# Kernel tuning notes

Measured on AMD Instinct MI355X. Metric: run time of the kernel, lower is better.

## Reference

```python
import jax, jax.numpy as jnp
import numpy as np

B, T, C = 2, 2048, 2048
H, HD = 16, 128          # n_head, head_dim
DC, DC1 = 672, 672        # kv / q compression dims
DR = 64                   # decoupled rope dim
DN = HD - DR              # nope dim = 64
GATE_CH = 32


def _rope(x, cos, sin):
    # x: (B,T,h,D); cos/sin: (B,T,D//2) -> broadcast over heads
    cos = cos[:, :, None, :]
    sin = sin[:, :, None, :]
    d = x.shape[-1] // 2
    x1, x2 = x[..., :d], x[..., d:]
    return jnp.concatenate([x1 * cos + x2 * sin, -x1 * sin + x2 * cos], axis=-1)


def _rmsnorm(x):
    eps = jnp.finfo(x.dtype).eps
    return x * jax.lax.rsqrt(jnp.mean(jnp.square(x), axis=-1, keepdims=True) + eps)


def setup_inputs() -> dict:
    key = jax.random.key(0)
    ks = jax.random.split(key, 10)
    x = jax.random.normal(ks[0], (B, T, C), jnp.float32)
    ve = jax.random.normal(ks[1], (B, T, H * HD), jnp.float32)
    # rotary tables for d_rope//2 = 32 frequencies
    inv_freq = 1.0 / (10000.0 ** (jnp.arange(DR // 2, dtype=jnp.float32) / (DR // 2)))
    ang = jnp.arange(T, dtype=jnp.float32)[:, None] * inv_freq[None, :]  # (T, DR//2)
    cos = jnp.broadcast_to(jnp.cos(ang)[None], (B, T, DR // 2)).astype(jnp.float32)
    sin = jnp.broadcast_to(jnp.sin(ang)[None], (B, T, DR // 2)).astype(jnp.float32)
    s = 0.02
    w_dkv = s * jax.random.normal(ks[2], (C, DC), jnp.float32)
    w_ukv = s * jax.random.normal(ks[3], (DC, H * (DN + HD)), jnp.float32)
    w_kr = s * jax.random.normal(ks[4], (C, DR), jnp.float32)
    w_dq = s * jax.random.normal(ks[5], (C, DC1), jnp.float32)
    w_q = s * jax.random.normal(ks[6], (DC1, H * HD), jnp.float32)
    w_cproj = s * jax.random.normal(ks[7], (H * HD, C), jnp.float32)
    w_ve_gate = s * jax.random.normal(ks[8], (GATE_CH, H), jnp.float32)
    return {"x": x, "ve": ve, "cos": cos, "sin": sin,
            "w_dkv": w_dkv, "w_ukv": w_ukv, "w_kr": w_kr, "w_dq": w_dq,
            "w_q": w_q, "w_cproj": w_cproj, "w_ve_gate": w_ve_gate,
            "window_size": 0}


def reference(x, ve, cos, sin, w_dkv, w_ukv, w_kr, w_dq, w_q, w_cproj, w_ve_gate, window_size):
    b, t, _ = x.shape
    # low-rank KV path
    c_kv = x @ w_dkv                                   # (B,T,DC)
    kv = (c_kv @ w_ukv).reshape(b, t, H, DN + HD)
    k_nope, v = kv[..., :DN], kv[..., DN:]
    # decoupled rope key (single shared head)
    k_rope = (x @ w_kr).reshape(b, t, 1, DR)
    k_rope = _rope(k_rope, cos, sin)
    # value-embedding gate
    gate = 2.0 * jax.nn.sigmoid(x[..., :GATE_CH] @ w_ve_gate)   # (B,T,H)
    v = v + gate[..., None] * ve.reshape(b, t, H, HD)
    # low-rank Q path
    q = ((x @ w_dq) @ w_q).reshape(b, t, H, HD)
    q_nope, q_rope = q[..., :DN], q[..., DN:]
    q_rope = _rope(q_rope, cos, sin)
    k = jnp.concatenate([k_nope, jnp.broadcast_to(k_rope, (b, t, H, DR))], axis=-1)
    q = jnp.concatenate([q_nope, q_rope], axis=-1)
    q, k = _rmsnorm(q), _rmsnorm(k)
    # causal attention (window_size==0 -> full causal, matching window_size=(-1,-1))
    scale = 1.0 / jnp.sqrt(jnp.float32(HD))
    scores = jnp.einsum('bqhd,bkhd->bhqk', q, k) * scale
    causal = jnp.tril(jnp.ones((t, t), dtype=bool))
    scores = jnp.where(causal[None, None], scores, jnp.finfo(scores.dtype).min)
    att = jax.nn.softmax(scores, axis=-1)
    y = jnp.einsum('bhqk,bkhd->bqhd', att, v).reshape(b, t, H * HD)
    return y @ w_cproj
```

## Files before the change

### kernel.cpp

```cpp
#include <hip/hip_runtime.h>
#include <hip/hip_bf16.h>

typedef unsigned short u16;
typedef unsigned int u32;
typedef __bf16 bf16x8 __attribute__((ext_vector_type(8)));
typedef float f32x4 __attribute__((ext_vector_type(4)));
typedef u16 ushort8 __attribute__((ext_vector_type(8)));

#define TSEQ 2048
#define NHEAD 16

#define GLD16(gp, lp) __builtin_amdgcn_global_load_lds( \
    (__attribute__((address_space(1))) void*)(gp), \
    (__attribute__((address_space(3))) void*)(lp), 16, 0, 0)

static __device__ __forceinline__ float bf2f(u16 u) {
  unsigned int x = ((unsigned int)u) << 16;
  union { unsigned int i; float f; } c; c.i = x; return c.f;
}
static __device__ __forceinline__ u16 f2bf(float f) {
  union { float f; unsigned int i; } c; c.f = f;
  unsigned int x = c.i;
  unsigned int r = (x + 0x7FFFu + ((x >> 16) & 1u)) >> 16;
  return (u16)r;
}
static __device__ __forceinline__ void st_out(u16* p, float v) { *p = f2bf(v); }
static __device__ __forceinline__ void st_out(float* p, float v) { *p = v; }
static __device__ __forceinline__ u32 cvtpk(float lo, float hi) {
  u32 w;
  asm("v_cvt_pk_bf16_f32 %0, %1, %2" : "=v"(w) : "v"(lo), "v"(hi));
  return w;
}

__global__ __launch_bounds__(256) void k_conv_x(const float* __restrict__ x, u16* __restrict__ xb) {
  size_t i = ((size_t)blockIdx.x * 256 + threadIdx.x) * 8;
  float4 a = *(const float4*)(x + i);
  float4 b = *(const float4*)(x + i + 4);
  ushort8 o;
  o[0] = f2bf(a.x); o[1] = f2bf(a.y); o[2] = f2bf(a.z); o[3] = f2bf(a.w);
  o[4] = f2bf(b.x); o[5] = f2bf(b.y); o[6] = f2bf(b.z); o[7] = f2bf(b.w);
  *(ushort8*)(xb + i) = o;
}

__global__ __launch_bounds__(256) void k_tconv_all(const float* __restrict__ w_dkv, const float* __restrict__ w_dq,
                                                   const float* __restrict__ w_kr, const float* __restrict__ w_ukv,
                                                   const float* __restrict__ w_q, const float* __restrict__ w_cp,
                                                   u16* __restrict__ wcatT, u16* __restrict__ wukvT,
                                                   u16* __restrict__ wqT, u16* __restrict__ wcpT) {
  __shared__ float sm[32][33];
  int z = blockIdx.x;
  const float* src; u16* dst; int R, Cc, Rpad, bx, by;
  if (z < 1536)       { src = w_dkv; dst = wcatT;              R = 2048; Cc = 672;  Rpad = 2048; int l = z;        bx = l % 64; by = l / 64; }
  else if (z < 3072)  { src = w_dq;  dst = wcatT + 768 * 2048; R = 2048; Cc = 672;  Rpad = 2048; int l = z - 1536; bx = l % 64; by = l / 64; }
  else if (z < 3200)  { src = w_kr;  dst = wcatT + 1536 * 2048;R = 2048; Cc = 64;   Rpad = 2048; int l = z - 3072; bx = l % 64; by = l / 64; }
  else if (z < 5504)  { src = w_ukv; dst = wukvT;              R = 672;  Cc = 3072; Rpad = 768;  int l = z - 3200; bx = l % 24; by = l / 24; }
  else if (z < 7040)  { src = w_q;   dst = wqT;                R = 672;  Cc = 2048; Rpad = 768;  int l = z - 5504; bx = l % 24; by = l / 24; }
  else                { src = w_cp;  dst = wcpT;               R = 2048; Cc = 2048; Rpad = 2048; int l = z - 7040; bx = l % 64; by = l / 64; }
  int tx = threadIdx.x & 31, ty = threadIdx.x >> 5;
  int r0 = bx * 32, c0 = by * 32;
#pragma unroll
  for (int i = 0; i < 4; i++) {
    int r = r0 + ty + 8 * i;
    int c = c0 + tx;
    sm[ty + 8 * i][tx] = (r < R && c < Cc) ? src[(size_t)r * Cc + c] : 0.f;
  }
  __syncthreads();
#pragma unroll
  for (int i = 0; i < 4; i++) {
    int c = c0 + ty + 8 * i;
    dst[(size_t)c * Rpad + r0 + tx] = f2bf(sm[tx][ty + 8 * i]);
  }
}

__global__ __launch_bounds__(256) void k_gate(const float* __restrict__ x, const float* __restrict__ wg,
                                              float* __restrict__ gate) {
  int idx = blockIdx.x * 256 + threadIdx.x;
  int m = idx >> 4, h = idx & 15;
  const float* xr = x + (size_t)m * 2048;
  float s = 0.f;
#pragma unroll
  for (int j = 0; j < 32; j++) s += xr[j] * wg[j * 16 + h];
  gate[idx] = 2.f / (1.f + __expf(-s));
}

template <typename OT>
__global__ __launch_bounds__(256) void k_gemm128(const u16* __restrict__ A, int lda,
                                                 const u16* __restrict__ BT, int ldb,
                                                 OT* __restrict__ C, int ldc,
                                                 int K) {
  __shared__ __align__(16) u16 As[128 * 32];
  __shared__ __align__(16) u16 Bs[128 * 32];
  int t = threadIdx.x;
  int wid = t >> 6, lane = t & 63;
  int m0 = blockIdx.y * 128, n0 = blockIdx.x * 128;
  int c0 = wid * 2;
  int srow0 = c0 * 16 + (lane >> 2);
  int scol = (lane & 3) * 8;
  const u16* Ag0 = A + (size_t)(m0 + srow0) * lda + scol;
  const u16* Ag1 = A + (size_t)(m0 + srow0 + 16) * lda + scol;
  const u16* Bg0 = BT + (size_t)(n0 + srow0) * ldb + scol;
  const u16* Bg1 = BT + (size_t)(n0 + srow0 + 16) * ldb + scol;
  u16* Al0 = &As[c0 * 512];
  u16* Al1 = &As[c0 * 512 + 512];
  u16* Bl0 = &Bs[c0 * 512];
  u16* Bl1 = &Bs[c0 * 512 + 512];
  int wr = (wid >> 1) * 64, wc = (wid & 1) * 64;
  int fr = lane & 15, fo = (lane >> 4) * 8;
  f32x4 acc[4][4];
#pragma unroll
  for (int m = 0; m < 4; m++)
#pragma unroll
    for (int n = 0; n < 4; n++) acc[m][n] = (f32x4){0, 0, 0, 0};
  for (int k0 = 0; k0 < K; k0 += 32) {
    GLD16(Ag0 + k0, Al0);
    GLD16(Ag1 + k0, Al1);
    GLD16(Bg0 + k0, Bl0);
    GLD16(Bg1 + k0, Bl1);
    __syncthreads();
    bf16x8 af[4], bf[4];
#pragma unroll
    for (int m = 0; m < 4; m++) af[m] = *(const bf16x8*)&As[(wr + m * 16 + fr) * 32 + fo];
#pragma unroll
    for (int n = 0; n < 4; n++) bf[n] = *(const bf16x8*)&Bs[(wc + n * 16 + fr) * 32 + fo];
#pragma unroll
    for (int m = 0; m < 4; m++)
#pragma unroll
      for (int n = 0; n < 4; n++)
        acc[m][n] = __builtin_amdgcn_mfma_f32_16x16x32_bf16(af[m], bf[n], acc[m][n], 0, 0, 0);
    __syncthreads();
  }
  int cr = (lane >> 4) * 4, cc = lane & 15;
#pragma unroll
  for (int m = 0; m < 4; m++)
#pragma unroll
    for (int n = 0; n < 4; n++)
#pragma unroll
      for (int r = 0; r < 4; r++)
        st_out(&C[(size_t)(m0 + wr + m * 16 + cr + r) * ldc + n0 + wc + n * 16 + cc], acc[m][n][r]);
}

__global__ __launch_bounds__(256) void k_gemm_dual(const u16* __restrict__ catout,
                                                   const u16* __restrict__ wukvT,
                                                   u16* __restrict__ kvb,
                                                   const u16* __restrict__ wqT,
                                                   const float* __restrict__ cosp,
                                                   const float* __restrict__ sinp,
                                                   u16* __restrict__ qf) {
  __shared__ __align__(16) u16 As[128 * 32];
  __shared__ __align__(16) u16 Bs[128 * 32];
  int t = threadIdx.x;
  int wid = t >> 6, lane = t & 63;
  int bx = blockIdx.x;
  bool isq = (bx >= 24);
  int nx = isq ? bx - 24 : bx;
  int m0 = blockIdx.y * 128, n0 = nx * 128;
  const u16* A = isq ? catout + 768 : catout;
  const u16* BT = isq ? wqT : wukvT;
  int c0 = wid * 2;
  int srow0 = c0 * 16 + (lane >> 2);
  int scol = (lane & 3) * 8;
  const u16* Ag0 = A + (size_t)(m0 + srow0) * 1664 + scol;
  const u16* Ag1 = A + (size_t)(m0 + srow0 + 16) * 1664 + scol;
  const u16* Bg0 = BT + (size_t)(n0 + srow0) * 768 + scol;
  const u16* Bg1 = BT + (size_t)(n0 + srow0 + 16) * 768 + scol;
  u16* Al0 = &As[c0 * 512];
  u16* Al1 = &As[c0 * 512 + 512];
  u16* Bl0 = &Bs[c0 * 512];
  u16* Bl1 = &Bs[c0 * 512 + 512];
  int wr = (wid >> 1) * 64, wc = (wid & 1) * 64;
  int fr = lane & 15, fo = (lane >> 4) * 8;
  f32x4 acc[4][4];
#pragma unroll
  for (int m = 0; m < 4; m++)
#pragma unroll
    for (int n = 0; n < 4; n++) acc[m][n] = (f32x4){0, 0, 0, 0};
  for (int k0 = 0; k0 < 768; k0 += 32) {
    GLD16(Ag0 + k0, Al0);
    GLD16(Ag1 + k0, Al1);
    GLD16(Bg0 + k0, Bl0);
    GLD16(Bg1 + k0, Bl1);
    __syncthreads();
    bf16x8 af[4], bf[4];
#pragma unroll
    for (int m = 0; m < 4; m++) af[m] = *(const bf16x8*)&As[(wr + m * 16 + fr) * 32 + fo];
#pragma unroll
    for (int n = 0; n < 4; n++) bf[n] = *(const bf16x8*)&Bs[(wc + n * 16 + fr) * 32 + fo];
#pragma unroll
    for (int m = 0; m < 4; m++)
#pragma unroll
      for (int n = 0; n < 4; n++)
        acc[m][n] = __builtin_amdgcn_mfma_f32_16x16x32_bf16(af[m], bf[n], acc[m][n], 0, 0, 0);
    __syncthreads();
  }
  int cr = (lane >> 4) * 4, cc = lane & 15;
  if (!isq) {
#pragma unroll
    for (int m = 0; m < 4; m++)
#pragma unroll
      for (int n = 0; n < 4; n++)
#pragma unroll
        for (int r = 0; r < 4; r++)
          kvb[(size_t)(m0 + wr + m * 16 + cr + r) * 3072 + n0 + wc + n * 16 + cc] = f2bf(acc[m][n][r]);
    return;
  }
  int h = nx;
  int wch = wid & 1;
  int wrg = wid >> 1;
  if (wch == 1) {
#pragma unroll
    for (int m = 0; m < 4; m++)
#pragma unroll
      for (int r = 0; r < 4; r++) {
        int grow = m0 + wr + m * 16 + cr + r;
#pragma unroll
        for (int n = 0; n < 2; n++) {
          int i = n * 16 + cc;
          float cth = cosp[(size_t)grow * 32 + i];
          float sth = sinp[(size_t)grow * 32 + i];
          float x1 = acc[m][n][r], x2 = acc[m][n + 2][r];
          acc[m][n][r]     = x1 * cth + x2 * sth;
          acc[m][n + 2][r] = x2 * cth - x1 * sth;
        }
      }
  }
  float part[4][4];
#pragma unroll
  for (int m = 0; m < 4; m++)
#pragma unroll
    for (int r = 0; r < 4; r++) {
      float s2 = 0.f;
#pragma unroll
      for (int n = 0; n < 4; n++) s2 += acc[m][n][r] * acc[m][n][r];
#pragma unroll
      for (int o = 1; o < 16; o <<= 1) s2 += __shfl_xor(s2, o, 64);
      part[m][r] = s2;
    }
  float* xs = (float*)As;
  if (cc == 0) {
#pragma unroll
    for (int m = 0; m < 4; m++)
#pragma unroll
      for (int r = 0; r < 4; r++)
        xs[(wrg * 2 + wch) * 64 + m * 16 + cr + r] = part[m][r];
  }
  __syncthreads();
#pragma unroll
  for (int m = 0; m < 4; m++)
#pragma unroll
    for (int r = 0; r < 4; r++) {
      int lrow = m * 16 + cr + r;
      float tot = part[m][r] + xs[(wrg * 2 + (wch ^ 1)) * 64 + lrow];
      float rms = rsqrtf(tot * (1.f / 128.f) + 1.1920929e-7f) * 0.1275174245f;
      int grow = m0 + wr + lrow;
      int b2 = grow >> 11, tt = grow & 2047;
      size_t base = (((size_t)(b2 * NHEAD + h)) * TSEQ + tt) * 128 + wch * 64;
#pragma unroll
      for (int n = 0; n < 4; n++)
        qf[base + n * 16 + cc] = f2bf(acc[m][n][r] * rms);
    }
}

__global__ __launch_bounds__(256) void k_build_k(const u16* __restrict__ kv, const u16* __restrict__ kr,
                                                 const float* __restrict__ cosp, const float* __restrict__ sinp,
                                                 u16* __restrict__ ksw) {
  __shared__ __align__(16) u16 sm[8192];
  int tid = threadIdx.x, wid = tid >> 6, lane = tid & 63;
  int bh = blockIdx.x >> 5, tile = blockIdx.x & 31;
  int b = bh >> 4, h = bh & 15;
  int d0 = lane * 2;
  for (int rr = 0; rr < 16; rr++) {
    int row = wid * 16 + rr;
    int t = tile * 64 + row;
    int m = b * TSEQ + t;
    float v[2];
#pragma unroll
    for (int e = 0; e < 2; e++) {
      int d = d0 + e;
      float val;
      if (d < 64) {
        val = bf2f(kv[(size_t)m * 3072 + h * 192 + d]);
      } else {
        int dd = d - 64, i = dd & 31;
        float c = cosp[m * 32 + i], s = sinp[m * 32 + i];
        float x1 = bf2f(kr[(size_t)m * 1664 + i]), x2 = bf2f(kr[(size_t)m * 1664 + 32 + i]);
        val = (dd < 32) ? (x1 * c + x2 * s) : (x2 * c - x1 * s);
      }
      v[e] = val;
    }
    float ss = v[0] * v[0] + v[1] * v[1];
#pragma unroll
    for (int o = 1; o < 64; o <<= 1) ss += __shfl_xor(ss, o, 64);
    float rms = rsqrtf(ss * (1.f / 128.f) + 1.1920929e-7f);
    int a = (row * 256 + d0 * 2) ^ ((row & 7) << 4);
    sm[a >> 1] = f2bf(v[0] * rms);
    sm[(a >> 1) + 1] = f2bf(v[1] * rms);
  }
  __syncthreads();
  u16* dst = ksw + ((size_t)(bh * 32 + tile)) * 8192 + tid * 32;
  const u16* src = sm + tid * 32;
#pragma unroll
  for (int j = 0; j < 4; j++)
    *(ushort8*)(dst + j * 8) = *(const ushort8*)(src + j * 8);
}

__global__ __launch_bounds__(256) void k_build_v(const u16* __restrict__ kv, const float* __restrict__ ve,
                                                 const float* __restrict__ gate, u16* __restrict__ vsw) {
  __shared__ __align__(16) char sm[128 * 128];
  int bh = blockIdx.x >> 5, tile = blockIdx.x & 31;
  int t0 = tile * 64;
  int b = bh >> 4, h = bh & 15;
  int tt = threadIdx.x >> 2, dp = (threadIdx.x & 3) * 32;
  int m = b * TSEQ + t0 + tt;
  float g = gate[m * 16 + h];
  const u16* kvp = kv + (size_t)m * 3072 + h * 192 + 64 + dp;
  const float* vep = ve + (size_t)m * 2048 + h * 128 + dp;
  ushort8 kvv[4];
  float4 vev[8];
#pragma unroll
  for (int u = 0; u < 4; u++) kvv[u] = *(const ushort8*)(kvp + u * 8);
#pragma unroll
  for (int u = 0; u < 8; u++) vev[u] = *(const float4*)(vep + u * 4);
#pragma unroll
  for (int j = 0; j < 32; j++) {
    float vvf = ((const float*)&vev[j >> 2])[j & 3];
    float v = bf2f(kvv[j >> 3][j & 7]) + g * vvf;
    int row = dp + j;
    int a = row * 128 + tt * 2;
    *(u16*)(sm + (a ^ ((row & 7) << 4))) = f2bf(v);
  }
  __syncthreads();
  u16* dst = vsw + ((size_t)(bh * 32 + tile)) * 8192 + threadIdx.x * 32;
  const u16* src = (const u16*)sm + threadIdx.x * 32;
#pragma unroll
  for (int j = 0; j < 4; j++)
    *(ushort8*)(dst + j * 8) = *(const ushort8*)(src + j * 8);
}

__global__ __launch_bounds__(256, 2) void k_attn(const u16* __restrict__ qf, const u16* __restrict__ ksw,
                                                 const u16* __restrict__ vsw, u16* __restrict__ y,
                                                 float* __restrict__ opart, float* __restrict__ mpart,
                                                 float* __restrict__ lpart) {
  __shared__ __align__(16) u16 kvbuf[2][2][8192];
  __shared__ __align__(16) char plds_all[4][4096];
  int tid = threadIdx.x, wid = tid >> 6, lane = tid & 63;
  int gq = lane >> 4, c = lane & 15;
  int xcd = blockIdx.x & 7, r0r = blockIdx.x >> 3;
  int bh, qb, it0, it1, pidx = -1;
  if (r0r < 64) {
    bh = xcd * 4 + (r0r & 3);
    int sub = r0r >> 2;
    qb = 15 - (sub >> 1);
    int half = sub & 1;
    it0 = half ? (qb + 1) : 0;
    it1 = half ? (2 * qb + 2) : (qb + 1);
    pidx = bh * 16 + (qb - 8) * 2 + half;
  } else {
    int rr = r0r - 64;
    bh = xcd * 4 + (rr & 3);
    qb = 7 - (rr >> 2);
    it0 = 0;
    it1 = 2 * qb + 2;
  }
  int q0w = qb * 128 + wid * 32;
  const u16* qp = qf + (size_t)bh * TSEQ * 128;
  const u16* kswb = ksw + (size_t)bh * 32 * 8192;
  const u16* vswb = vsw + (size_t)bh * 32 * 8192;
  char* plds = plds_all[wid];
  int swz = (c & 7) << 4;
  bf16x8 qfr[2][4];
#pragma unroll
  for (int rg = 0; rg < 2; rg++)
#pragma unroll
    for (int kc = 0; kc < 4; kc++)
      qfr[rg][kc] = *(const bf16x8*)(qp + (size_t)(q0w + rg * 16 + c) * 128 + kc * 32 + gq * 8);
  f32x4 oacc[2][8];
#pragma unroll
  for (int rg = 0; rg < 2; rg++)
#pragma unroll
    for (int nd = 0; nd < 8; nd++) oacc[rg][nd] = (f32x4){0, 0, 0, 0};
  float mreg[2] = {-1e30f, -1e30f}, lreg[2] = {0.f, 0.f};
  int chunk = wid * 4;
#pragma unroll
  for (int j = 0; j < 4; j++) {
    GLD16(kswb + (size_t)it0 * 8192 + (chunk + j) * 512 + lane * 8, &kvbuf[0][0][(chunk + j) * 512]);
    GLD16(vswb + (size_t)it0 * 8192 + (chunk + j) * 512 + lane * 8, &kvbuf[0][1][(chunk + j) * 512]);
  }
  __syncthreads();
  for (int it = it0; it < it1; it++) {
    int cur = (it - it0) & 1;
    if (it + 1 < it1) {
      const u16* kt = kswb + (size_t)(it + 1) * 8192;
      const u16* vt = vswb + (size_t)(it + 1) * 8192;
#pragma unroll
      for (int j = 0; j < 4; j++) {
        GLD16(kt + (chunk + j) * 512 + lane * 8, &kvbuf[cur ^ 1][0][(chunk + j) * 512]);
        GLD16(vt + (chunk + j) * 512 + lane * 8, &kvbuf[cur ^ 1][1][(chunk + j) * 512]);
      }
    }
    int kt0 = it * 64;
    if (kt0 <= q0w + 31) {
      const char* Kt = (const char*)kvbuf[cur][0];
      const char* Vt = (const char*)kvbuf[cur][1];
      bool maskit = (kt0 + 63 > q0w);
      f32x4 sacc[2][4];
#pragma unroll
      for (int rg = 0; rg < 2; rg++)
#pragma unroll
        for (int s = 0; s < 4; s++) sacc[rg][s] = (f32x4){0, 0, 0, 0};
#pragma unroll
      for (int s = 0; s < 4; s++) {
        int row = s * 16 + c;
#pragma unroll
        for (int kc = 0; kc < 4; kc++) {
          int a = (row * 256 + (kc * 32 + gq * 8) * 2) ^ ((row & 7) << 4);
          bf16x8 kfr = *(const bf16x8*)(Kt + a);
          sacc[0][s] = __builtin_amdgcn_mfma_f32_16x16x32_bf16(kfr, qfr[0][kc], sacc[0][s], 0, 0, 0);
          sacc[1][s] = __builtin_amdgcn_mfma_f32_16x16x32_bf16(kfr, qfr[1][kc], sacc[1][s], 0, 0, 0);
        }
      }
      if (maskit) {
#pragma unroll
        for (int rg = 0; rg < 2; rg++) {
          int qrow = q0w + rg * 16 + c;
#pragma unroll
          for (int s = 0; s < 4; s++)
#pragma unroll
            for (int r = 0; r < 4; r++) {
              int key = kt0 + s * 16 + gq * 4 + r;
              sacc[rg][s][r] = (key <= qrow) ? sacc[rg][s][r] : -3e38f;
            }
        }
      }
      float mx[2];
#pragma unroll
      for (int rg = 0; rg < 2; rg++) {
        float m2 = sacc[rg][0][0];
#pragma unroll
        for (int s = 0; s < 4; s++)
#pragma unroll
          for (int r = 0; r < 4; r++) m2 = fmaxf(m2, sacc[rg][s][r]);
        m2 = fmaxf(m2, __shfl_xor(m2, 16, 64));
        m2 = fmaxf(m2, __shfl_xor(m2, 32, 64));
        mx[rg] = m2;
      }
      bool ok = (mx[0] - mreg[0] <= 11.f) && (mx[1] - mreg[1] <= 11.f);
      if (!__all(ok)) {
#pragma unroll
        for (int rg = 0; rg < 2; rg++) {
          float mn = fmaxf(mreg[rg], mx[rg]);
          float fac = exp2f(mreg[rg] - mn);
          lreg[rg] *= fac;
          float fq[4];
#pragma unroll
          for (int r = 0; r < 4; r++) fq[r] = __shfl(fac, gq * 4 + r, 64);
#pragma unroll
          for (int nd = 0; nd < 8; nd++)
#pragma unroll
            for (int r = 0; r < 4; r++) oacc[rg][nd][r] *= fq[r];
          mreg[rg] = mn;
        }
      }
#pragma unroll
      for (int rg = 0; rg < 2; rg++) {
        float p[4][4];
        float rs = 0.f;
#pragma unroll
        for (int s = 0; s < 4; s++)
#pragma unroll
          for (int r = 0; r < 4; r++) {
            p[s][r] = exp2f(sacc[rg][s][r] - mreg[rg]);
            rs += p[s][r];
          }
        rs += __shfl_xor(rs, 16, 64);
        rs += __shfl_xor(rs, 32, 64);
        lreg[rg] += rs;
#pragma unroll
        for (int s = 0; s < 4; s++) {
          u32 w0 = cvtpk(p[s][0], p[s][1]);
          u32 w1 = cvtpk(p[s][2], p[s][3]);
          int a = (rg * 2048 + c * 128 + s * 32 + gq * 8) ^ swz;
          *(uint2*)(plds + a) = make_uint2(w0, w1);
        }
      }
#pragma unroll
      for (int kc2 = 0; kc2 < 2; kc2++) {
        int a0 = (c * 128 + kc2 * 64 + gq * 16) ^ swz;
        bf16x8 pa0 = *(const bf16x8*)(plds + a0);
        bf16x8 pa1 = *(const bf16x8*)(plds + 2048 + a0);
#pragma unroll
        for (int nd = 0; nd < 8; nd++) {
          int vrow = nd * 16 + c;
          int av = (vrow * 128 + (kc2 * 32 + gq * 8) * 2) ^ ((vrow & 7) << 4);
          bf16x8 vfr = *(const bf16x8*)(Vt + av);
          oacc[0][nd] = __builtin_amdgcn_mfma_f32_16x16x32_bf16(pa0, vfr, oacc[0][nd], 0, 0, 0);
          oacc[1][nd] = __builtin_amdgcn_mfma_f32_16x16x32_bf16(pa1, vfr, oacc[1][nd], 0, 0, 0);
        }
      }
    }
    __syncthreads();
  }
  if (pidx >= 0) {
    float* op = opart + (size_t)pidx * 16384;
#pragma unroll
    for (int rg = 0; rg < 2; rg++) {
#pragma unroll
      for (int nd = 0; nd < 8; nd++)
#pragma unroll
        for (int r = 0; r < 4; r++)
          op[(wid * 32 + rg * 16 + gq * 4 + r) * 128 + nd * 16 + c] = oacc[rg][nd][r];
      if (gq == 0) {
        mpart[pidx * 128 + wid * 32 + rg * 16 + c] = mreg[rg];
        lpart[pidx * 128 + wid * 32 + rg * 16 + c] = lreg[rg];
      }
    }
    return;
  }
  int b2 = bh >> 4, h2 = bh & 15;
#pragma unroll
  for (int rg = 0; rg < 2; rg++) {
    float linv = 1.f / lreg[rg];
    float inv[4];
#pragma unroll
    for (int r = 0; r < 4; r++) inv[r] = __shfl(linv, gq * 4 + r, 64);
#pragma unroll
    for (int nd = 0; nd < 8; nd++) {
#pragma unroll
      for (int r = 0; r < 4; r++) {
        size_t offo = ((size_t)(b2 * TSEQ + q0w + rg * 16 + gq * 4 + r)) * 2048 + h2 * 128 + nd * 16 + c;
        y[offo] = f2bf(oacc[rg][nd][r] * inv[r]);
      }
    }
  }
}

__global__ __launch_bounds__(256) void k_merge(const float* __restrict__ opart, const float* __restrict__ mpart,
                                               const float* __restrict__ lpart, u16* __restrict__ y) {
  int blk = blockIdx.x;
  int bh = blk >> 3, qb = 8 + (blk & 7);
  int p0 = bh * 16 + (qb - 8) * 2, p1 = p0 + 1;
  int b2 = bh >> 4, h2 = bh & 15;
  for (int e = threadIdx.x; e < 16384; e += 256) {
    int row = e >> 7, col = e & 127;
    float m0 = mpart[p0 * 128 + row], m1 = mpart[p1 * 128 + row];
    float mm = fmaxf(m0, m1);
    float e0 = exp2f(m0 - mm), e1 = exp2f(m1 - mm);
    float l = lpart[p0 * 128 + row] * e0 + lpart[p1 * 128 + row] * e1;
    float o = opart[(size_t)p0 * 16384 + row * 128 + col] * e0 +
              opart[(size_t)p1 * 16384 + row * 128 + col] * e1;
    y[((size_t)(b2 * TSEQ + qb * 128 + row)) * 2048 + h2 * 128 + col] = f2bf(o / l);
  }
}

extern "C" void kernel_launch(void* const* d_in, const int* in_sizes, int n_in,
                              void* d_out, int out_size, void* d_ws, size_t ws_size,
                              hipStream_t stream) {
  (void)in_sizes; (void)n_in; (void)out_size; (void)ws_size;
  const float* x      = (const float*)d_in[0];
  const float* ve     = (const float*)d_in[1];
  const float* cosp   = (const float*)d_in[2];
  const float* sinp   = (const float*)d_in[3];
  const float* w_dkv  = (const float*)d_in[4];
  const float* w_ukv  = (const float*)d_in[5];
  const float* w_kr   = (const float*)d_in[6];
  const float* w_dq   = (const float*)d_in[7];
  const float* w_q    = (const float*)d_in[8];
  const float* w_cp   = (const float*)d_in[9];
  const float* w_vg   = (const float*)d_in[10];
  float* out = (float*)d_out;

  char* ws = (char*)d_ws;
  size_t off = 0;
  auto alloc = [&](size_t bytes) -> char* {
    char* p = ws + off;
    off += (bytes + 255) & ~(size_t)255;
    return p;
  };
  u16* xb     = (u16*)alloc(4096ull * 2048 * 2);
  u16* wcatT  = (u16*)alloc(1664ull * 2048 * 2);
  u16* wukvT  = (u16*)alloc(3072ull * 768 * 2);
  u16* wqT    = (u16*)alloc(2048ull * 768 * 2);
  u16* wcpT   = (u16*)alloc(2048ull * 2048 * 2);
  u16* catout = (u16*)alloc(4096ull * 1664 * 2);
  u16* kvb    = (u16*)alloc(4096ull * 3072 * 2);
  float* gateb = (float*)alloc(4096ull * 16 * 4);
  u16* qfb    = (u16*)alloc(2ull * 16 * 2048 * 128 * 2);
  u16* kswb   = (u16*)alloc(32ull * 32 * 8192 * 2);
  u16* vswb   = (u16*)alloc(32ull * 32 * 8192 * 2);
  u16* yb = xb;
  float* opart = (float*)catout;
  float* mpart = opart + 512 * 16384;
  float* lpart = mpart + 512 * 128;

  k_conv_x<<<dim3(4096), dim3(256), 0, stream>>>(x, xb);
  k_tconv_all<<<dim3(11136), dim3(256), 0, stream>>>(w_dkv, w_dq, w_kr, w_ukv, w_q, w_cp,
                                                     wcatT, wukvT, wqT, wcpT);
  k_gate<<<dim3(256), dim3(256), 0, stream>>>(x, w_vg, gateb);

  k_gemm128<u16><<<dim3(13, 32), dim3(256), 0, stream>>>(xb, 2048, wcatT, 2048, catout, 1664, 2048);
  k_gemm_dual<<<dim3(40, 32), dim3(256), 0, stream>>>(catout, wukvT, kvb, wqT, cosp, sinp, qfb);

  k_build_k<<<dim3(1024), dim3(256), 0, stream>>>(kvb, catout + 1536, cosp, sinp, kswb);
  k_build_v<<<dim3(1024), dim3(256), 0, stream>>>(kvb, ve, gateb, vswb);

  k_attn<<<dim3(768), dim3(256), 0, stream>>>(qfb, kswb, vswb, yb, opart, mpart, lpart);
  k_merge<<<dim3(256), dim3(256), 0, stream>>>(opart, mpart, lpart, yb);

  k_gemm128<float><<<dim3(16, 32), dim3(256), 0, stream>>>(yb, 2048, wcpT, 2048, out, 2048, 2048);
}
```

Before: 346.1 us.

## Halve attention KV tile to 32 keys, raise occupancy, rebalance split work

The attention kernel now streams 32-key K/V sub-tiles instead of 64, which halves its LDS footprint and lets launch bounds target 4 blocks per CU. The K/V builders write each 64-row tile as two 32-row halves so the layout matches. The split-KV scheme is extended from 8 to 12 query blocks, with a new grid of 896 blocks and a merge grid of 384. Partial buffers move to the weight region to fit the larger split count. The cost is more loop iterations and barriers per key, with less MFMA work per iteration.

```diff
diff --git a/kernel.cpp b/kernel.cpp
--- a/kernel.cpp
+++ b/kernel.cpp
@@ -291,7 +291,7 @@
 #pragma unroll
     for (int o = 1; o < 64; o <<= 1) ss += __shfl_xor(ss, o, 64);
     float rms = rsqrtf(ss * (1.f / 128.f) + 1.1920929e-7f);
-    int a = (row * 256 + d0 * 2) ^ ((row & 7) << 4);
+    int a = ((row & 32) ? 8192 : 0) + (((row & 31) * 256 + d0 * 2) ^ ((row & 7) << 4));
     sm[a >> 1] = f2bf(v[0] * rms);
     sm[(a >> 1) + 1] = f2bf(v[1] * rms);
   }
@@ -320,13 +320,14 @@
   for (int u = 0; u < 4; u++) kvv[u] = *(const ushort8*)(kvp + u * 8);
 #pragma unroll
   for (int u = 0; u < 8; u++) vev[u] = *(const float4*)(vep + u * 4);
+  int half = (tt >> 5) * 8192, tloc = tt & 31;
 #pragma unroll
   for (int j = 0; j < 32; j++) {
     float vvf = ((const float*)&vev[j >> 2])[j & 3];
     float v = bf2f(kvv[j >> 3][j & 7]) + g * vvf;
     int row = dp + j;
-    int a = row * 128 + tt * 2;
-    *(u16*)(sm + (a ^ ((row & 7) << 4))) = f2bf(v);
+    int a = half + ((row * 64 + tloc * 2) ^ ((row & 7) << 4));
+    *(u16*)(sm + a) = f2bf(v);
   }
   __syncthreads();
   u16* dst = vsw + ((size_t)(bh * 32 + tile)) * 8192 + threadIdx.x * 32;
@@ -336,30 +337,29 @@
     *(ushort8*)(dst + j * 8) = *(const ushort8*)(src + j * 8);
 }
 
-__global__ __launch_bounds__(256, 2) void k_attn(const u16* __restrict__ qf, const u16* __restrict__ ksw,
+__global__ __launch_bounds__(256, 4) void k_attn(const u16* __restrict__ qf, const u16* __restrict__ ksw,
                                                  const u16* __restrict__ vsw, u16* __restrict__ y,
                                                  float* __restrict__ opart, float* __restrict__ mpart,
                                                  float* __restrict__ lpart) {
-  __shared__ __align__(16) u16 kvbuf[2][2][8192];
-  __shared__ __align__(16) char plds_all[4][4096];
+  __shared__ __align__(16) u16 kvbuf[2][2][4096];
+  __shared__ __align__(16) char plds_all[4][2048];
   int tid = threadIdx.x, wid = tid >> 6, lane = tid & 63;
   int gq = lane >> 4, c = lane & 15;
-  int xcd = blockIdx.x & 7, r0r = blockIdx.x >> 3;
-  int bh, qb, it0, it1, pidx = -1;
-  if (r0r < 64) {
-    bh = xcd * 4 + (r0r & 3);
-    int sub = r0r >> 2;
+  int xcd = blockIdx.x & 7, idx = blockIdx.x >> 3;
+  int bh = xcd * 4 + (idx & 3);
+  int sub = idx >> 2;
+  int qb, it0, it1, pidx = -1;
+  if (sub < 24) {
     qb = 15 - (sub >> 1);
     int half = sub & 1;
-    it0 = half ? (qb + 1) : 0;
-    it1 = half ? (2 * qb + 2) : (qb + 1);
-    pidx = bh * 16 + (qb - 8) * 2 + half;
+    int nhalf = 2 * qb + 2;
+    it0 = half * nhalf;
+    it1 = it0 + nhalf;
+    pidx = bh * 24 + (qb - 4) * 2 + half;
   } else {
-    int rr = r0r - 64;
-    bh = xcd * 4 + (rr & 3);
-    qb = 7 - (rr >> 2);
+    qb = 27 - sub;
     it0 = 0;
-    it1 = 2 * qb + 2;
+    it1 = 4 * qb + 4;
   }
   int q0w = qb * 128 + wid * 32;
   const u16* qp = qf + (size_t)bh * TSEQ * 128;
@@ -379,36 +379,36 @@
 #pragma unroll
     for (int nd = 0; nd < 8; nd++) oacc[rg][nd] = (f32x4){0, 0, 0, 0};
   float mreg[2] = {-1e30f, -1e30f}, lreg[2] = {0.f, 0.f};
-  int chunk = wid * 4;
-#pragma unroll
-  for (int j = 0; j < 4; j++) {
-    GLD16(kswb + (size_t)it0 * 8192 + (chunk + j) * 512 + lane * 8, &kvbuf[0][0][(chunk + j) * 512]);
-    GLD16(vswb + (size_t)it0 * 8192 + (chunk + j) * 512 + lane * 8, &kvbuf[0][1][(chunk + j) * 512]);
+  int ch = wid * 2;
+#pragma unroll
+  for (int j = 0; j < 2; j++) {
+    GLD16(kswb + (size_t)it0 * 4096 + (ch + j) * 512 + lane * 8, &kvbuf[0][0][(ch + j) * 512]);
+    GLD16(vswb + (size_t)it0 * 4096 + (ch + j) * 512 + lane * 8, &kvbuf[0][1][(ch + j) * 512]);
   }
   __syncthreads();
   for (int it = it0; it < it1; it++) {
     int cur = (it - it0) & 1;
     if (it + 1 < it1) {
-      const u16* kt = kswb + (size_t)(it + 1) * 8192;
-      const u16* vt = vswb + (size_t)(it + 1) * 8192;
-#pragma unroll
-      for (int j = 0; j < 4; j++) {
-        GLD16(kt + (chunk + j) * 512 + lane * 8, &kvbuf[cur ^ 1][0][(chunk + j) * 512]);
-        GLD16(vt + (chunk + j) * 512 + lane * 8, &kvbuf[cur ^ 1][1][(chunk + j) * 512]);
+      const u16* kt = kswb + (size_t)(it + 1) * 4096;
+      const u16* vt = vswb + (size_t)(it + 1) * 4096;
+#pragma unroll
+      for (int j = 0; j < 2; j++) {
+        GLD16(kt + (ch + j) * 512 + lane * 8, &kvbuf[cur ^ 1][0][(ch + j) * 512]);
+        GLD16(vt + (ch + j) * 512 + lane * 8, &kvbuf[cur ^ 1][1][(ch + j) * 512]);
       }
     }
-    int kt0 = it * 64;
+    int kt0 = it * 32;
     if (kt0 <= q0w + 31) {
       const char* Kt = (const char*)kvbuf[cur][0];
       const char* Vt = (const char*)kvbuf[cur][1];
-      bool maskit = (kt0 + 63 > q0w);
-      f32x4 sacc[2][4];
+      bool maskit = (kt0 + 31 > q0w);
+      f32x4 sacc[2][2];
 #pragma unroll
       for (int rg = 0; rg < 2; rg++)
 #pragma unroll
-        for (int s = 0; s < 4; s++) sacc[rg][s] = (f32x4){0, 0, 0, 0};
-#pragma unroll
-      for (int s = 0; s < 4; s++) {
+        for (int s = 0; s < 2; s++) sacc[rg][s] = (f32x4){0, 0, 0, 0};
+#pragma unroll
+      for (int s = 0; s < 2; s++) {
         int row = s * 16 + c;
 #pragma unroll
         for (int kc = 0; kc < 4; kc++) {
@@ -423,7 +423,7 @@
         for (int rg = 0; rg < 2; rg++) {
           int qrow = q0w + rg * 16 + c;
 #pragma unroll
-          for (int s = 0; s < 4; s++)
+          for (int s = 0; s < 2; s++)
 #pragma unroll
             for (int r = 0; r < 4; r++) {
               int key = kt0 + s * 16 + gq * 4 + r;
@@ -436,7 +436,7 @@
       for (int rg = 0; rg < 2; rg++) {
         float m2 = sacc[rg][0][0];
 #pragma unroll
-        for (int s = 0; s < 4; s++)
+        for (int s = 0; s < 2; s++)
 #pragma unroll
           for (int r = 0; r < 4; r++) m2 = fmaxf(m2, sacc[rg][s][r]);
         m2 = fmaxf(m2, __shfl_xor(m2, 16, 64));
@@ -462,10 +462,10 @@
       }
 #pragma unroll
       for (int rg = 0; rg < 2; rg++) {
-        float p[4][4];
+        float p[2][4];
         float rs = 0.f;
 #pragma unroll
-        for (int s = 0; s < 4; s++)
+        for (int s = 0; s < 2; s++)
 #pragma unroll
           for (int r = 0; r < 4; r++) {
             p[s][r] = exp2f(sacc[rg][s][r] - mreg[rg]);
@@ -475,22 +475,21 @@
         rs += __shfl_xor(rs, 32, 64);
         lreg[rg] += rs;
 #pragma unroll
-        for (int s = 0; s < 4; s++) {
+        for (int s = 0; s < 2; s++) {
           u32 w0 = cvtpk(p[s][0], p[s][1]);
           u32 w1 = cvtpk(p[s][2], p[s][3]);
-          int a = (rg * 2048 + c * 128 + s * 32 + gq * 8) ^ swz;
+          int a = (rg * 1024 + ((c * 64 + s * 32 + gq * 8) ^ swz));
           *(uint2*)(plds + a) = make_uint2(w0, w1);
         }
       }
-#pragma unroll
-      for (int kc2 = 0; kc2 < 2; kc2++) {
-        int a0 = (c * 128 + kc2 * 64 + gq * 16) ^ swz;
+      {
+        int a0 = (c * 64 + gq * 16) ^ swz;
         bf16x8 pa0 = *(const bf16x8*)(plds + a0);
-        bf16x8 pa1 = *(const bf16x8*)(plds + 2048 + a0);
+        bf16x8 pa1 = *(const bf16x8*)(plds + 1024 + a0);
 #pragma unroll
         for (int nd = 0; nd < 8; nd++) {
           int vrow = nd * 16 + c;
-          int av = (vrow * 128 + (kc2 * 32 + gq * 8) * 2) ^ ((vrow & 7) << 4);
+          int av = (vrow * 64 + gq * 16) ^ ((vrow & 7) << 4);
           bf16x8 vfr = *(const bf16x8*)(Vt + av);
           oacc[0][nd] = __builtin_amdgcn_mfma_f32_16x16x32_bf16(pa0, vfr, oacc[0][nd], 0, 0, 0);
           oacc[1][nd] = __builtin_amdgcn_mfma_f32_16x16x32_bf16(pa1, vfr, oacc[1][nd], 0, 0, 0);
@@ -536,8 +535,8 @@
 __global__ __launch_bounds__(256) void k_merge(const float* __restrict__ opart, const float* __restrict__ mpart,
                                                const float* __restrict__ lpart, u16* __restrict__ y) {
   int blk = blockIdx.x;
-  int bh = blk >> 3, qb = 8 + (blk & 7);
-  int p0 = bh * 16 + (qb - 8) * 2, p1 = p0 + 1;
+  int bh = blk / 12, qq = blk % 12, qb = 4 + qq;
+  int p0 = bh * 24 + qq * 2, p1 = p0 + 1;
   int b2 = bh >> 4, h2 = bh & 15;
   for (int e = threadIdx.x; e < 16384; e += 256) {
     int row = e >> 7, col = e & 127;
@@ -576,20 +575,20 @@
     return p;
   };
   u16* xb     = (u16*)alloc(4096ull * 2048 * 2);
-  u16* wcatT  = (u16*)alloc(1664ull * 2048 * 2);
-  u16* wukvT  = (u16*)alloc(3072ull * 768 * 2);
-  u16* wqT    = (u16*)alloc(2048ull * 768 * 2);
   u16* wcpT   = (u16*)alloc(2048ull * 2048 * 2);
-  u16* catout = (u16*)alloc(4096ull * 1664 * 2);
-  u16* kvb    = (u16*)alloc(4096ull * 3072 * 2);
   float* gateb = (float*)alloc(4096ull * 16 * 4);
   u16* qfb    = (u16*)alloc(2ull * 16 * 2048 * 128 * 2);
   u16* kswb   = (u16*)alloc(32ull * 32 * 8192 * 2);
   u16* vswb   = (u16*)alloc(32ull * 32 * 8192 * 2);
+  u16* wcatT  = (u16*)alloc(1664ull * 2048 * 2);
+  u16* wukvT  = (u16*)alloc(3072ull * 768 * 2);
+  u16* wqT    = (u16*)alloc(2048ull * 768 * 2);
+  u16* catout = (u16*)alloc(4096ull * 1664 * 2);
+  u16* kvb    = (u16*)alloc(4096ull * 3072 * 2);
   u16* yb = xb;
-  float* opart = (float*)catout;
-  float* mpart = opart + 512 * 16384;
-  float* lpart = mpart + 512 * 128;
+  float* opart = (float*)wcatT;
+  float* mpart = opart + 768 * 16384;
+  float* lpart = mpart + 768 * 128;
 
   k_conv_x<<<dim3(4096), dim3(256), 0, stream>>>(x, xb);
   k_tconv_all<<<dim3(11136), dim3(256), 0, stream>>>(w_dkv, w_dq, w_kr, w_ukv, w_q, w_cp,
@@ -602,8 +601,8 @@
   k_build_k<<<dim3(1024), dim3(256), 0, stream>>>(kvb, catout + 1536, cosp, sinp, kswb);
   k_build_v<<<dim3(1024), dim3(256), 0, stream>>>(kvb, ve, gateb, vswb);
 
-  k_attn<<<dim3(768), dim3(256), 0, stream>>>(qfb, kswb, vswb, yb, opart, mpart, lpart);
-  k_merge<<<dim3(256), dim3(256), 0, stream>>>(opart, mpart, lpart, yb);
+  k_attn<<<dim3(896), dim3(256), 0, stream>>>(qfb, kswb, vswb, yb, opart, mpart, lpart);
+  k_merge<<<dim3(384), dim3(256), 0, stream>>>(opart, mpart, lpart, yb);
 
   k_gemm128<float><<<dim3(16, 32), dim3(256), 0, stream>>>(yb, 2048, wcpT, 2048, out, 2048, 2048);
 }
```

After: 529.6 us. 1.53x slower.
